# Kernel tuning notes

Measured on AMD Instinct MI355X. Metric: run time of the kernel, lower is better.

The kernel has to match this reference:

```python
import jax, jax.numpy as jnp
import numpy as np

B, T, M, D, H, DFF = 8, 512, 64, 1024, 16, 4096
DH = D // H          # 64 head dim
ROT = DH // 2        # 32 rotary dims (int(head_dim*0.5))
ROPE_BASE = 10000.0
LN_EPS = 1e-5


def layernorm(x, g, b):
    mu = jnp.mean(x, -1, keepdims=True)
    var = jnp.mean(jnp.square(x - mu), -1, keepdims=True)
    return (x - mu) * jax.lax.rsqrt(var + LN_EPS) * g + b


def rotate_half(x):
    x1, x2 = x[..., : x.shape[-1] // 2], x[..., x.shape[-1] // 2:]
    return jnp.concatenate((-x2, x1), -1)


def setup_inputs() -> dict:
    key = jax.random.key(0)
    ks = jax.random.split(key, 8)
    s = 0.02
    return {
        "x": jax.random.normal(ks[0], (B, T, D), jnp.float32),
        "memory": jax.random.normal(ks[1], (B, M, D), jnp.float32),
        "Wq": jax.random.normal(ks[2], (D, D), jnp.float32) * s,
        "bq": jnp.zeros((D,), jnp.float32),
        "Wk": jax.random.normal(ks[3], (D, D), jnp.float32) * s,
        "bk": jnp.zeros((D,), jnp.float32),
        "Wv": jax.random.normal(ks[4], (D, D), jnp.float32) * s,
        "bv": jnp.zeros((D,), jnp.float32),
        "Wo": jax.random.normal(ks[5], (D, D), jnp.float32) * s,
        "bo": jnp.zeros((D,), jnp.float32),
        "W1": jax.random.normal(ks[6], (DFF, D), jnp.float32) * s,
        "b1": jnp.zeros((DFF,), jnp.float32),
        "W2": jax.random.normal(ks[7], (D, DFF), jnp.float32) * s,
        "b2": jnp.zeros((D,), jnp.float32),
        "g_attn": jnp.ones((D,), jnp.float32),
        "beta_attn": jnp.zeros((D,), jnp.float32),
        "g_mlp": jnp.ones((D,), jnp.float32),
        "beta_mlp": jnp.zeros((D,), jnp.float32),
    }


def reference(x, memory, Wq, bq, Wk, bk, Wv, bv, Wo, bo, W1, b1, W2, b2,
              g_attn, beta_attn, g_mlp, beta_mlp):
    L = M + T
    x_full = jnp.concatenate([memory, x], axis=1)            # (B, L, D)
    xa = layernorm(x_full, g_attn, beta_attn)

    def heads(t):  # (B, L, D) -> (B, H, L, DH)
        return t.reshape(B, L, H, DH).transpose(0, 2, 1, 3)

    q = heads(xa @ Wq.T + bq)
    k = heads(xa @ Wk.T + bk)
    v = heads(xa @ Wv.T + bv)

    # partial rotary embedding on first ROT dims
    inv_freq = 1.0 / (ROPE_BASE ** (jnp.arange(0, ROT, 2, dtype=jnp.float32) / ROT))
    freqs = jnp.arange(L, dtype=jnp.float32)[:, None] * inv_freq[None, :]  # (L, ROT/2)
    emb = jnp.concatenate((freqs, freqs), -1)                # (L, ROT)
    cos = jnp.cos(emb)[None, None]                           # (1,1,L,ROT)
    sin = jnp.sin(emb)[None, None]
    q_rot, q_pass = q[..., :ROT], q[..., ROT:]
    k_rot, k_pass = k[..., :ROT], k[..., ROT:]
    q_rot = q_rot * cos + rotate_half(q_rot) * sin
    k_rot = k_rot * cos + rotate_half(k_rot) * sin
    q = jnp.concatenate((q_rot, q_pass), -1)
    k = jnp.concatenate((k_rot, k_pass), -1)

    # prompt mask: memory rows attend memory only; target rows attend memory + causal target
    idx = jnp.arange(L)
    row, col = idx[:, None], idx[None, :]
    allowed = (col < M) | ((row >= M) & (col <= row))        # (L, L) bool

    scores = jnp.einsum('bhqd,bhkd->bhqk', q, k) / jnp.sqrt(jnp.float32(DH))
    scores = jnp.where(allowed[None, None], scores, jnp.float32(-1e30))
    attn = jax.nn.softmax(scores, axis=-1)
    o = jnp.einsum('bhqk,bhkd->bhqd', attn, v)
    o = o.transpose(0, 2, 1, 3).reshape(B, L, D)
    x_full = x_full + (o @ Wo.T + bo)

    xn = layernorm(x_full, g_mlp, beta_mlp)
    h = jnp.square(jax.nn.relu(xn @ W1.T + b1))              # ReLU^2 FFN
    x_full = x_full + (h @ W2.T + b2)
    return x_full[:, M:]
```

## Files before the change

### kernel.cpp

```cpp
#include <hip/hip_runtime.h>
#include <hip/hip_bf16.h>
#include <cmath>

using bf16 = __hip_bfloat16;
typedef __attribute__((ext_vector_type(8))) __bf16 bf16x8;
typedef __attribute__((ext_vector_type(4))) float f32x4;

struct __align__(8) bf16x4s { bf16 a, b, c, d; };

__device__ inline void gload_lds16(const void* g, void* l) {
  __builtin_amdgcn_global_load_lds(
      (__attribute__((address_space(1))) void*)g,
      (__attribute__((address_space(3))) void*)l, 16, 0, 0);
}

__device__ inline f32x4 mfma16(bf16x8 a, bf16x8 b, f32x4 c) {
  return __builtin_amdgcn_mfma_f32_16x16x32_bf16(a, b, c, 0, 0, 0);
}

#define BAR() __builtin_amdgcn_s_barrier()
#define VMC(N) asm volatile("s_waitcnt vmcnt(" #N ")" ::: "memory")
#define LGKM0() asm volatile("s_waitcnt lgkmcnt(0)" ::: "memory")

template<int MODE, int CHUNK>
__global__ __launch_bounds__(512) void gemm256(
    const bf16* __restrict__ A, int lda, long sA,
    const bf16* __restrict__ B, int ldb, long sB,
    const float* __restrict__ bias,
    void* __restrict__ Out,
    int K, int ldo, long zstride)
{
  __shared__ bf16 lds[65536];
  const int tid = threadIdx.x, lane = tid & 63, wid = tid >> 6;
  const int wr = wid >> 2, wc = wid & 3;
  const int gx = gridDim.x;
  const int bidl = blockIdx.x + gx * blockIdx.y;
  const int xcd = bidl & 7, slot = bidl >> 3;
  int bx, by;
  if constexpr (CHUNK == 0) {
    const int sx = gx >> 2, sy = gridDim.y >> 1;
    bx = (xcd & 3) * sx + slot % sx;
    by = (xcd >> 2) * sy + slot / sx;
  } else {
    bx = slot % gx;
    by = xcd * (gridDim.y >> 3) + slot / gx;
  }
  const int m0 = by * 256, n0 = bx * 256;
  const int z = blockIdx.z;
  const bf16* Ab = A + (long)z * sA;
  const bf16* Bb = B + (long)z * sB;
  const int nt = K >> 6;

  f32x4 acc[8][4] = {};

  auto STAGE = [&](int par, int t, int part) {
    const bf16* src = (part < 2) ? Ab : Bb;
    const int ld = (part < 2) ? lda : ldb;
    const int rb = ((part < 2) ? m0 : n0) + (part & 1) * 128;
    const int k0 = t << 6;
    bf16* dst = &lds[(par * 4 + part) * 8192];
#pragma unroll
    for (int j = 0; j < 2; ++j) {
      int idx = j * 512 + tid;
      int row = idx >> 3;
      int ce = ((idx & 7) ^ (row & 7)) << 3;
      gload_lds16(src + (long)(rb + row) * ld + k0 + ce, dst + idx * 8);
    }
  };
  auto load_a = [&](bf16x8 (&a_)[4][2], int par, int mh) {
#pragma unroll
    for (int mf = 0; mf < 4; ++mf)
#pragma unroll
      for (int kk = 0; kk < 2; ++kk) {
        int r = mh * 64 + mf * 16 + (lane & 15);
        int cb = (kk * 64 + ((lane >> 4) << 4)) ^ ((r & 7) << 4);
        a_[mf][kk] = *(const bf16x8*)&lds[(par * 4 + wr) * 8192 + r * 64 + (cb >> 1)];
      }
  };
  auto load_b = [&](bf16x8 (&b_)[2][2], int par, int nh) {
#pragma unroll
    for (int nf = 0; nf < 2; ++nf)
#pragma unroll
      for (int kk = 0; kk < 2; ++kk) {
        int r = (wc & 1) * 64 + (nh * 2 + nf) * 16 + (lane & 15);
        int cb = (kk * 64 + ((lane >> 4) << 4)) ^ ((r & 7) << 4);
        b_[nf][kk] = *(const bf16x8*)&lds[(par * 4 + 2 + (wc >> 1)) * 8192 + r * 64 + (cb >> 1)];
      }
  };
  auto qmfma = [&](bf16x8 (&a_)[4][2], bf16x8 (&b_)[2][2], int mh, int nh) {
    __builtin_amdgcn_s_setprio(1);
#pragma unroll
    for (int mf = 0; mf < 4; ++mf)
#pragma unroll
      for (int nf = 0; nf < 2; ++nf)
#pragma unroll
        for (int kk = 0; kk < 2; ++kk)
          acc[mh * 4 + mf][nh * 2 + nf] =
              mfma16(a_[mf][kk], b_[nf][kk], acc[mh * 4 + mf][nh * 2 + nf]);
    __builtin_amdgcn_s_setprio(0);
  };

  STAGE(0, 0, 0); STAGE(0, 0, 1); STAGE(0, 0, 2); STAGE(0, 0, 3);
  STAGE(1, 1, 2); STAGE(1, 1, 0);
  VMC(4);
  BAR();

  const int half = nt >> 1;
  for (int i = 0; i < half; ++i) {
    const int u = 2 * i;
    const bool full = (i < half - 1);
    bf16x8 a[4][2], b0[2][2], b1[2][2];
    load_a(a, 0, 0); load_b(b0, 0, 0);
    STAGE(1, u + 1, 3);
    BAR();
    qmfma(a, b0, 0, 0);
    BAR();
    load_b(b1, 0, 1);
    STAGE(1, u + 1, 1);
    BAR();
    qmfma(a, b1, 0, 1);
    BAR();
    load_a(a, 0, 1);
    if (full) STAGE(0, u + 2, 2);
    BAR();
    qmfma(a, b1, 1, 1);
    BAR();
    if (full) STAGE(0, u + 2, 0);
    BAR();
    qmfma(a, b0, 1, 0);
    if (full) { VMC(4); } else { VMC(0); }
    BAR();
    load_a(a, 1, 0); load_b(b0, 1, 0);
    if (full) STAGE(0, u + 2, 3);
    BAR();
    qmfma(a, b0, 0, 0);
    BAR();
    load_b(b1, 1, 1);
    if (full) STAGE(0, u + 2, 1);
    BAR();
    qmfma(a, b1, 0, 1);
    BAR();
    load_a(a, 1, 1);
    if (full) STAGE(1, u + 3, 2);
    BAR();
    qmfma(a, b1, 1, 1);
    BAR();
    if (full) STAGE(1, u + 3, 0);
    BAR();
    qmfma(a, b0, 1, 0);
    if (full) VMC(4);
    BAR();
  }

  const int cb0 = n0 + wc * 64 + (lane & 15);
  const int rb0 = m0 + wr * 128 + ((lane >> 4) << 2);
#pragma unroll
  for (int mf = 0; mf < 8; ++mf) {
#pragma unroll
    for (int nf = 0; nf < 4; ++nf) {
      int c = cb0 + nf * 16;
#pragma unroll
      for (int j = 0; j < 4; ++j) {
        int rr = rb0 + mf * 16 + j;
        float v = acc[mf][nf][j];
        if constexpr (MODE == 0) {
          ((bf16*)Out)[(long)rr * ldo + c] = __float2bfloat16(v + bias[c]);
        } else if constexpr (MODE == 2) {
          float t2 = fmaxf(v + bias[c], 0.0f);
          ((bf16*)Out)[(long)rr * ldo + c] = __float2bfloat16(t2 * t2);
        } else {
          ((bf16*)Out)[(long)z * zstride + (long)rr * ldo + c] = __float2bfloat16(v);
        }
      }
    }
  }
}

__global__ __launch_bounds__(256) void reduce_k(
    const bf16* __restrict__ part, const float* __restrict__ bias,
    const float* __restrict__ resid, float* __restrict__ out)
{
  const int row = blockIdx.x, tid = threadIdx.x;
  const long rb = (long)row * 1024 + tid * 4;
  float a0 = 0, a1 = 0, a2 = 0, a3 = 0;
#pragma unroll
  for (int z = 0; z < 4; ++z) {
    bf16x4s t = *(const bf16x4s*)(part + (long)z * 4194304 + rb);
    a0 += __bfloat162float(t.a); a1 += __bfloat162float(t.b);
    a2 += __bfloat162float(t.c); a3 += __bfloat162float(t.d);
  }
  float4 b = ((const float4*)bias)[tid];
  float4 r = *(const float4*)(resid + rb);
  float4 o;
  o.x = a0 + b.x + r.x; o.y = a1 + b.y + r.y;
  o.z = a2 + b.z + r.z; o.w = a3 + b.w + r.w;
  *(float4*)(out + rb) = o;
}

__global__ __launch_bounds__(256) void reduce_ln(
    const bf16* __restrict__ part, const float* __restrict__ bias,
    const float* __restrict__ resid, const float* __restrict__ g,
    const float* __restrict__ beta, float* __restrict__ x2,
    bf16* __restrict__ xn)
{
  const int row = blockIdx.x, tid = threadIdx.x;
  const long rb = (long)row * 1024 + tid * 4;
  float a0 = 0, a1 = 0, a2 = 0, a3 = 0;
#pragma unroll
  for (int z = 0; z < 4; ++z) {
    bf16x4s t = *(const bf16x4s*)(part + (long)z * 4194304 + rb);
    a0 += __bfloat162float(t.a); a1 += __bfloat162float(t.b);
    a2 += __bfloat162float(t.c); a3 += __bfloat162float(t.d);
  }
  float4 bb4 = ((const float4*)bias)[tid];
  float4 rr4 = *(const float4*)(resid + rb);
  float4 v;
  v.x = a0 + bb4.x + rr4.x; v.y = a1 + bb4.y + rr4.y;
  v.z = a2 + bb4.z + rr4.z; v.w = a3 + bb4.w + rr4.w;
  *(float4*)(x2 + rb) = v;

  float s = v.x + v.y + v.z + v.w;
  float s2 = v.x * v.x + v.y * v.y + v.z * v.z + v.w * v.w;
#pragma unroll
  for (int o = 32; o; o >>= 1) {
    s += __shfl_down(s, o);
    s2 += __shfl_down(s2, o);
  }
  __shared__ float red[8];
  const int w = tid >> 6, lane = tid & 63;
  if (lane == 0) { red[w] = s; red[4 + w] = s2; }
  __syncthreads();
  float S = red[0] + red[1] + red[2] + red[3];
  float S2 = red[4] + red[5] + red[6] + red[7];
  float mu = S * (1.0f / 1024.0f);
  float rs = rsqrtf(S2 * (1.0f / 1024.0f) - mu * mu + 1e-5f);
  float4 gg = ((const float4*)g)[tid];
  float4 be = ((const float4*)beta)[tid];
  bf16x4s o4;
  o4.a = __float2bfloat16((v.x - mu) * rs * gg.x + be.x);
  o4.b = __float2bfloat16((v.y - mu) * rs * gg.y + be.y);
  o4.c = __float2bfloat16((v.z - mu) * rs * gg.z + be.z);
  o4.d = __float2bfloat16((v.w - mu) * rs * gg.w + be.w);
  *(bf16x4s*)(xn + rb) = o4;
}

__global__ __launch_bounds__(256) void flash_attn(
    const bf16* __restrict__ qh, const bf16* __restrict__ kh,
    const bf16* __restrict__ vt, bf16* __restrict__ attn)
{
  __shared__ bf16 ks[2][64 * 64];
  __shared__ bf16 vs[2][64 * 64];
  __shared__ bf16 pq[64 * 64];
  const int tid = threadIdx.x, lane = tid & 63, wv = tid >> 6;
  const int bid = blockIdx.x;
  const int xcd = bid & 7, sl = bid >> 3;
  const int zh = xcd * 16 + (sl >> 3);
  const int qt = sl & 7;
  const int b = zh >> 4, h = zh & 15;
  const int q0 = qt * 64;
  const bf16* qb = qh + (long)zh * 32768 + (long)q0 * 64;
  const bf16* kb = kh + (long)zh * 36864;
  const bf16* vb = vt + (long)zh * 36864;

#pragma unroll
  for (int i = 0; i < 2; ++i) {
    int idx = i * 256 + tid;
    int row = idx >> 3;
    int ce = ((idx & 7) ^ (row & 7)) << 3;
    gload_lds16(qb + (long)row * 64 + ce, pq + idx * 8);
  }
  auto stage_kv = [&](int bb, int j) {
#pragma unroll
    for (int it = 0; it < 2; ++it) {
      int idx = it * 256 + tid;
      int row = idx >> 3;
      int ce = ((idx & 7) ^ (row & 7)) << 3;
      gload_lds16(kb + (long)(j * 64 + row) * 64 + ce, &ks[bb][idx * 8]);
    }
#pragma unroll
    for (int it = 0; it < 2; ++it) {
      int idx = it * 256 + tid;
      int row = idx >> 3;
      int ce = ((idx & 7) ^ (row & 7)) << 3;
      gload_lds16(vb + (long)row * 576 + j * 64 + ce, &vs[bb][idx * 8]);
    }
  };
  stage_kv(0, 0);
  VMC(0);
  BAR();

  bf16x8 qf[2];
  {
    int r = wv * 16 + (lane & 15);
#pragma unroll
    for (int kk = 0; kk < 2; ++kk) {
      int c0 = kk * 32 + ((lane >> 4) << 3);
      qf[kk] = *(const bf16x8*)&pq[r * 64 + (c0 ^ ((r & 7) << 3))];
    }
  }

  f32x4 acc_o[4] = {};
  float mrun[4], lrun[4];
#pragma unroll
  for (int jj = 0; jj < 4; ++jj) { mrun[jj] = -1e30f; lrun[jj] = 0.0f; }

  const int nkv = qt + 2;
  int cur = 0;
  for (int j = 0; j < nkv; ++j) {
    if (j + 1 < nkv) stage_kv(cur ^ 1, j + 1);

    f32x4 sv[4] = {};
    __builtin_amdgcn_s_setprio(1);
#pragma unroll
    for (int kk = 0; kk < 2; ++kk) {
      bf16x8 kf[4];
      int c0 = kk * 32 + ((lane >> 4) << 3);
#pragma unroll
      for (int n = 0; n < 4; ++n) {
        int r = n * 16 + (lane & 15);
        kf[n] = *(const bf16x8*)&ks[cur][r * 64 + (c0 ^ ((r & 7) << 3))];
      }
#pragma unroll
      for (int n = 0; n < 4; ++n) sv[n] = mfma16(qf[kk], kf[n], sv[n]);
    }
    __builtin_amdgcn_s_setprio(0);

    if (j == nkv - 1) {
#pragma unroll
      for (int n = 0; n < 4; ++n) {
        int c = n * 16 + (lane & 15);
#pragma unroll
        for (int jj = 0; jj < 4; ++jj) {
          int r = wv * 16 + ((lane >> 4) << 2) + jj;
          if (c > r) sv[n][jj] = -1e30f;
        }
      }
    }
#pragma unroll
    for (int jj = 0; jj < 4; ++jj) {
      float pm = fmaxf(fmaxf(sv[0][jj], sv[1][jj]), fmaxf(sv[2][jj], sv[3][jj]));
#pragma unroll
      for (int off = 1; off < 16; off <<= 1) pm = fmaxf(pm, __shfl_xor(pm, off));
      float mnew = fmaxf(mrun[jj], pm);
      float sc = exp2f(mrun[jj] - mnew);
      mrun[jj] = mnew;
      float rs = 0.0f;
#pragma unroll
      for (int n = 0; n < 4; ++n) {
        float p = exp2f(sv[n][jj] - mnew);
        sv[n][jj] = p;
        rs += p;
      }
#pragma unroll
      for (int off = 1; off < 16; off <<= 1) rs += __shfl_xor(rs, off);
      lrun[jj] = lrun[jj] * sc + rs;
#pragma unroll
      for (int nd = 0; nd < 4; ++nd) acc_o[nd][jj] *= sc;
    }
#pragma unroll
    for (int n = 0; n < 4; ++n)
#pragma unroll
      for (int jj = 0; jj < 4; ++jj) {
        int pr = wv * 16 + ((lane >> 4) << 2) + jj;
        int pc = n * 16 + (lane & 15);
        pq[pr * 64 + (pc ^ ((pr & 7) << 3))] = __float2bfloat16(sv[n][jj]);
      }
    __builtin_amdgcn_s_setprio(1);
#pragma unroll
    for (int kk = 0; kk < 2; ++kk) {
      int c0 = kk * 32 + ((lane >> 4) << 3);
      bf16x8 pa, vf[4];
      {
        int r = wv * 16 + (lane & 15);
        pa = *(const bf16x8*)&pq[r * 64 + (c0 ^ ((r & 7) << 3))];
      }
#pragma unroll
      for (int nd = 0; nd < 4; ++nd) {
        int r = nd * 16 + (lane & 15);
        vf[nd] = *(const bf16x8*)&vs[cur][r * 64 + (c0 ^ ((r & 7) << 3))];
      }
#pragma unroll
      for (int nd = 0; nd < 4; ++nd) acc_o[nd] = mfma16(pa, vf[nd], acc_o[nd]);
    }
    __builtin_amdgcn_s_setprio(0);

    if (j + 1 < nkv) {
      LGKM0();
      VMC(0);
      BAR();
      cur ^= 1;
    }
  }
  bf16* ob = attn + ((long)b * 512 + q0) * 1024 + h * 64;
#pragma unroll
  for (int jj = 0; jj < 4; ++jj) {
    float inv = 1.0f / lrun[jj];
    int r = wv * 16 + ((lane >> 4) << 2) + jj;
#pragma unroll
    for (int nd = 0; nd < 4; ++nd)
      ob[(long)r * 1024 + nd * 16 + (lane & 15)] = __float2bfloat16(acc_o[nd][jj] * inv);
  }
}

template<bool CONCAT>
__global__ __launch_bounds__(256) void ln_kernel(
    const float* __restrict__ xin, const float* __restrict__ mem,
    const float* __restrict__ g, const float* __restrict__ beta,
    bf16* __restrict__ out)
{
  const int row = blockIdx.x;
  const float* src;
  if (CONCAT) {
    int b = row / 576, p = row % 576;
    src = (p < 64) ? (mem + ((long)b * 64 + p) * 1024)
                   : (xin + ((long)b * 512 + (p - 64)) * 1024);
  } else {
    src = xin + (long)row * 1024;
  }
  const int tid = threadIdx.x;
  float4 v = ((const float4*)src)[tid];
  float s = v.x + v.y + v.z + v.w;
  float s2 = v.x * v.x + v.y * v.y + v.z * v.z + v.w * v.w;
#pragma unroll
  for (int o = 32; o; o >>= 1) {
    s += __shfl_down(s, o);
    s2 += __shfl_down(s2, o);
  }
  __shared__ float red[8];
  const int w = tid >> 6, lane = tid & 63;
  if (lane == 0) { red[w] = s; red[4 + w] = s2; }
  __syncthreads();
  float S = red[0] + red[1] + red[2] + red[3];
  float S2 = red[4] + red[5] + red[6] + red[7];
  float mu = S * (1.0f / 1024.0f);
  float rs = rsqrtf(S2 * (1.0f / 1024.0f) - mu * mu + 1e-5f);
  float4 gg = ((const float4*)g)[tid];
  float4 bb = ((const float4*)beta)[tid];
  bf16x4s o4;
  o4.a = __float2bfloat16((v.x - mu) * rs * gg.x + bb.x);
  o4.b = __float2bfloat16((v.y - mu) * rs * gg.y + bb.y);
  o4.c = __float2bfloat16((v.z - mu) * rs * gg.z + bb.z);
  o4.d = __float2bfloat16((v.w - mu) * rs * gg.w + bb.w);
  *(bf16x4s*)(out + (long)row * 1024 + tid * 4) = o4;
}

__global__ __launch_bounds__(256) void cvt_weights(
    const float* __restrict__ wq, const float* __restrict__ wk,
    const float* __restrict__ wv, const float* __restrict__ wo,
    const float* __restrict__ w1, const float* __restrict__ w2,
    bf16* __restrict__ out)
{
  long e = ((long)blockIdx.x * 256 + threadIdx.x) * 4;
  const long DD = 1048576, DF = 4194304;
  const float* src; long base;
  if (e < DD)            { src = wq; base = 0; }
  else if (e < 2 * DD)   { src = wk; base = DD; }
  else if (e < 3 * DD)   { src = wv; base = 2 * DD; }
  else if (e < 4 * DD)   { src = wo; base = 3 * DD; }
  else if (e < 4 * DD + DF) { src = w1; base = 4 * DD; }
  else                   { src = w2; base = 4 * DD + DF; }
  float4 v = *(const float4*)(src + (e - base));
  bf16x4s o4;
  o4.a = __float2bfloat16(v.x);
  o4.b = __float2bfloat16(v.y);
  o4.c = __float2bfloat16(v.z);
  o4.d = __float2bfloat16(v.w);
  *(bf16x4s*)(out + e) = o4;
}

__global__ __launch_bounds__(256) void bias_concat(
    const float* __restrict__ bq, const float* __restrict__ bk,
    const float* __restrict__ bv, float* __restrict__ out)
{
  int i = blockIdx.x * 256 + threadIdx.x;
  if (i < 1024)      out[i] = bq[i];
  else if (i < 2048) out[i] = bk[i - 1024];
  else if (i < 3072) out[i] = bv[i - 2048];
}

__global__ __launch_bounds__(256) void rope_tab_kernel(float* __restrict__ tab)
{
  int i = blockIdx.x * 256 + threadIdx.x;
  if (i >= 9216) return;
  int p = i >> 4, f = i & 15;
  float invf = expf(-(float)f * 0.5756462732485114f);
  float ang = (float)p * invf;
  tab[i] = cosf(ang);
  tab[9216 + i] = sinf(ang);
}

__global__ __launch_bounds__(256) void rope_reshape(
    const bf16* __restrict__ qkv, const float* __restrict__ tab,
    bf16* __restrict__ qh, bf16* __restrict__ kh, bf16* __restrict__ vt)
{
  const float QSCALE = 0.18033688011112043f;
  long i = (long)blockIdx.x * 256 + threadIdx.x;
  if (i >= 8L * 576 * 1024) return;
  int dfull = (int)(i & 1023);
  long bp = i >> 10;
  int p = (int)(bp % 576);
  int b = (int)(bp / 576);
  int h = dfull >> 6, d = dfull & 63;
  const bf16* rowp = qkv + bp * 3072;

  float cosv = 1.0f, sinv = 0.0f;
  const bool rot = d < 32;
  int pd = 0;
  if (rot) {
    int i0 = d & 15;
    cosv = tab[p * 16 + i0];
    sinv = tab[9216 + p * 16 + i0];
    pd = (d < 16) ? d + 16 : d - 16;
  }
  {
    float v0 = __bfloat162float(rowp[1024 + dfull]);
    float ov = v0;
    if (rot) {
      float v1 = __bfloat162float(rowp[1024 + (h << 6) + pd]);
      ov = (d < 16) ? (v0 * cosv - v1 * sinv) : (v0 * cosv + v1 * sinv);
    }
    kh[(((long)b * 16 + h) * 576 + p) * 64 + d] = __float2bfloat16(ov);
  }
  vt[(((long)b * 16 + h) * 64 + d) * 576 + p] = rowp[2048 + dfull];
  if (p >= 64) {
    float v0 = __bfloat162float(rowp[dfull]);
    float ov = v0;
    if (rot) {
      float v1 = __bfloat162float(rowp[(h << 6) + pd]);
      ov = (d < 16) ? (v0 * cosv - v1 * sinv) : (v0 * cosv + v1 * sinv);
    }
    qh[(((long)b * 16 + h) * 512 + (p - 64)) * 64 + d] = __float2bfloat16(ov * QSCALE);
  }
}

extern "C" void kernel_launch(void* const* d_in, const int* in_sizes, int n_in,
                              void* d_out, int out_size, void* d_ws, size_t ws_size,
                              hipStream_t stream)
{
  (void)in_sizes; (void)n_in; (void)out_size; (void)ws_size;
  const float* x    = (const float*)d_in[0];
  const float* mem  = (const float*)d_in[1];
  const float* Wq   = (const float*)d_in[2];
  const float* bq   = (const float*)d_in[3];
  const float* Wk   = (const float*)d_in[4];
  const float* bk   = (const float*)d_in[5];
  const float* Wv   = (const float*)d_in[6];
  const float* bv   = (const float*)d_in[7];
  const float* Wo   = (const float*)d_in[8];
  const float* bo   = (const float*)d_in[9];
  const float* W1   = (const float*)d_in[10];
  const float* b1   = (const float*)d_in[11];
  const float* W2   = (const float*)d_in[12];
  const float* b2   = (const float*)d_in[13];
  const float* g_a  = (const float*)d_in[14];
  const float* bt_a = (const float*)d_in[15];
  const float* g_m  = (const float*)d_in[16];
  const float* bt_m = (const float*)d_in[17];
  float* out = (float*)d_out;

  char* ws = (char*)d_ws;
  size_t off = 0;
  auto carve = [&](size_t bytes) -> void* {
    void* p = ws + off;
    off = (off + bytes + 255) & ~(size_t)255;
    return p;
  };
  bf16*  wB    = (bf16*)carve(12582912L * 2);
  float* bqkv  = (float*)carve(3072 * 4);
  float* rtab  = (float*)carve(9216 * 2 * 4);
  bf16*  xa    = (bf16*)carve(4608L * 1024 * 2);
  bf16*  qkv   = (bf16*)carve(4608L * 3072 * 2);
  bf16*  qh    = (bf16*)carve(8L * 16 * 512 * 64 * 2);
  bf16*  kh    = (bf16*)carve(8L * 16 * 576 * 64 * 2);
  bf16*  vt    = (bf16*)carve(8L * 16 * 576 * 64 * 2);
  bf16*  attn  = (bf16*)carve(4096L * 1024 * 2);
  float* x2    = (float*)carve(4096L * 1024 * 4);
  bf16*  xn    = (bf16*)carve(4096L * 1024 * 2);
  bf16*  hbuf  = (bf16*)carve(4096L * 4096 * 2);
  bf16*  partsb= (bf16*)carve(4L * 4096 * 1024 * 2);

  cvt_weights<<<12288, 256, 0, stream>>>(Wq, Wk, Wv, Wo, W1, W2, wB);
  bias_concat<<<12, 256, 0, stream>>>(bq, bk, bv, bqkv);
  rope_tab_kernel<<<36, 256, 0, stream>>>(rtab);
  ln_kernel<true><<<4608, 256, 0, stream>>>(x, mem, g_a, bt_a, xa);

  gemm256<0, 0><<<dim3(12, 18, 1), 512, 0, stream>>>(
      xa, 1024, 0, wB, 1024, 0, bqkv, qkv, 1024, 3072, 0);

  rope_reshape<<<18432, 256, 0, stream>>>(qkv, rtab, qh, kh, vt);

  flash_attn<<<1024, 256, 0, stream>>>(qh, kh, vt, attn);

  gemm256<8, 1><<<dim3(4, 16, 4), 512, 0, stream>>>(
      attn, 1024, 256, wB + 3145728L, 1024, 256, nullptr, partsb, 256, 1024, 4194304L);
  reduce_ln<<<4096, 256, 0, stream>>>(partsb, bo, x, g_m, bt_m, x2, xn);

  gemm256<2, 0><<<dim3(16, 16, 1), 512, 0, stream>>>(
      xn, 1024, 0, wB + 4194304L, 1024, 0, b1, hbuf, 1024, 4096, 0);

  gemm256<8, 1><<<dim3(4, 16, 4), 512, 0, stream>>>(
      hbuf, 4096, 1024, wB + 8388608L, 4096, 1024, nullptr, partsb, 1024, 1024, 4194304L);
  reduce_k<<<4096, 256, 0, stream>>>(partsb, b2, x2, out);
}
```

Baseline: 241.9 us.

## Fuse RoPE and head reshape into QKV GEMM epilogue, stage stores through LDS

The QKV projection GEMM now applies bias, rotary embedding and the Q scale in its epilogue and writes Q, K and row-major V straight into per-head layouts. This drops the intermediate qkv buffer and the separate rope_reshape pass. A small tiled v_transpose kernel then produces the transposed V. All GEMM epilogues now stage results through swizzled LDS and emit 16-byte vector stores instead of scattered 2-byte stores. The cost is extra LDS traffic and a barrier in the epilogue, plus one added kernel launch.

```diff
diff --git a/kernel.cpp b/kernel.cpp
--- a/kernel.cpp
+++ b/kernel.cpp
@@ -28,22 +28,24 @@
     const bf16* __restrict__ B, int ldb, long sB,
     const float* __restrict__ bias,
     void* __restrict__ Out,
-    int K, int ldo, long zstride)
+    int K, int ldo, long zstride,
+    const float* __restrict__ rtab,
+    bf16* __restrict__ o1, bf16* __restrict__ o2, bf16* __restrict__ o3)
 {
   __shared__ bf16 lds[65536];
   const int tid = threadIdx.x, lane = tid & 63, wid = tid >> 6;
   const int wr = wid >> 2, wc = wid & 3;
   const int gx = gridDim.x;
   const int bidl = blockIdx.x + gx * blockIdx.y;
-  const int xcd = bidl & 7, slot = bidl >> 3;
+  const int xcd = bidl & 7, slot_ = bidl >> 3;
   int bx, by;
   if constexpr (CHUNK == 0) {
     const int sx = gx >> 2, sy = gridDim.y >> 1;
-    bx = (xcd & 3) * sx + slot % sx;
-    by = (xcd >> 2) * sy + slot / sx;
+    bx = (xcd & 3) * sx + slot_ % sx;
+    by = (xcd >> 2) * sy + slot_ / sx;
   } else {
-    bx = slot % gx;
-    by = xcd * (gridDim.y >> 3) + slot / gx;
+    bx = slot_ % gx;
+    by = xcd * (gridDim.y >> 3) + slot_ / gx;
   }
   const int m0 = by * 256, n0 = bx * 256;
   const int z = blockIdx.z;
@@ -152,26 +154,74 @@
     BAR();
   }
 
-  const int cb0 = n0 + wc * 64 + (lane & 15);
-  const int rb0 = m0 + wr * 128 + ((lane >> 4) << 2);
+  bf16* slot = &lds[wid * 8192];
+  const int l15 = lane & 15;
+  const int matq = n0 >> 10;
+  const int hh = ((n0 & 1023) >> 6) + wc;
+  float b0v = 0, b1v = 0, b2v = 0, b3v = 0;
+  if constexpr (MODE != 8) {
+    b0v = bias[n0 + wc * 64 + l15];
+    b1v = bias[n0 + wc * 64 + l15 + 16];
+    b2v = bias[n0 + wc * 64 + l15 + 32];
+    b3v = bias[n0 + wc * 64 + l15 + 48];
+  }
 #pragma unroll
   for (int mf = 0; mf < 8; ++mf) {
 #pragma unroll
-    for (int nf = 0; nf < 4; ++nf) {
-      int c = cb0 + nf * 16;
-#pragma unroll
-      for (int j = 0; j < 4; ++j) {
-        int rr = rb0 + mf * 16 + j;
-        float v = acc[mf][nf][j];
-        if constexpr (MODE == 0) {
-          ((bf16*)Out)[(long)rr * ldo + c] = __float2bfloat16(v + bias[c]);
-        } else if constexpr (MODE == 2) {
-          float t2 = fmaxf(v + bias[c], 0.0f);
-          ((bf16*)Out)[(long)rr * ldo + c] = __float2bfloat16(t2 * t2);
-        } else {
-          ((bf16*)Out)[(long)z * zstride + (long)rr * ldo + c] = __float2bfloat16(v);
+    for (int j = 0; j < 4; ++j) {
+      int lr = mf * 16 + ((lane >> 4) << 2) + j;
+      float a0 = acc[mf][0][j] + b0v;
+      float a1 = acc[mf][1][j] + b1v;
+      float a2 = acc[mf][2][j] + b2v;
+      float a3 = acc[mf][3][j] + b3v;
+      if constexpr (MODE == 9) {
+        if (matq < 2) {
+          int rr = m0 + wr * 128 + lr;
+          int p = rr % 576;
+          float cs = rtab[p * 16 + l15];
+          float sn = rtab[9216 + p * 16 + l15];
+          float r0 = a0 * cs - a1 * sn;
+          float r1 = a1 * cs + a0 * sn;
+          a0 = r0; a1 = r1;
+          if (matq == 0) {
+            const float QS = 0.18033688011112043f;
+            a0 *= QS; a1 *= QS; a2 *= QS; a3 *= QS;
+          }
         }
-      }
+      } else if constexpr (MODE == 2) {
+        a0 = fmaxf(a0, 0.f); a0 *= a0;
+        a1 = fmaxf(a1, 0.f); a1 *= a1;
+        a2 = fmaxf(a2, 0.f); a2 *= a2;
+        a3 = fmaxf(a3, 0.f); a3 *= a3;
+      }
+      int sw = (lr & 7) << 3;
+      slot[lr * 64 + ((l15) ^ sw)]        = __float2bfloat16(a0);
+      slot[lr * 64 + ((l15 + 16) ^ sw)]   = __float2bfloat16(a1);
+      slot[lr * 64 + ((l15 + 32) ^ sw)]   = __float2bfloat16(a2);
+      slot[lr * 64 + ((l15 + 48) ^ sw)]   = __float2bfloat16(a3);
+    }
+  }
+  __syncthreads();
+#pragma unroll
+  for (int it = 0; it < 16; ++it) {
+    int u = it * 64 + lane;
+    int r_s = u >> 3, c_s = u & 7;
+    int rr = m0 + wr * 128 + r_s;
+    bf16x8 val = *(const bf16x8*)&slot[r_s * 64 + ((c_s ^ (r_s & 7)) << 3)];
+    if constexpr (MODE == 9) {
+      int b_ = rr / 576, p = rr - b_ * 576;
+      int zh = b_ * 16 + hh;
+      if (matq == 0) {
+        if (p >= 64)
+          *(bf16x8*)(o1 + ((long)zh * 512 + (p - 64)) * 64 + c_s * 8) = val;
+      } else if (matq == 1) {
+        *(bf16x8*)(o2 + ((long)zh * 576 + p) * 64 + c_s * 8) = val;
+      } else {
+        *(bf16x8*)(o3 + ((long)zh * 576 + p) * 64 + c_s * 8) = val;
+      }
+    } else {
+      long zoff = (MODE == 8) ? (long)z * zstride : 0;
+      *(bf16x8*)((bf16*)Out + zoff + (long)rr * ldo + n0 + wc * 64 + c_s * 8) = val;
     }
   }
 }
@@ -244,6 +294,32 @@
   *(bf16x4s*)(xn + rb) = o4;
 }
 
+__global__ __launch_bounds__(256) void v_transpose(
+    const bf16* __restrict__ vrow, bf16* __restrict__ vt)
+{
+  __shared__ bf16 t[64][72];
+  const int tid = threadIdx.x;
+  const int zh = blockIdx.y, pb = blockIdx.x;
+  const bf16* src = vrow + ((long)zh * 576 + pb * 64) * 64;
+#pragma unroll
+  for (int it = 0; it < 2; ++it) {
+    int idx = it * 256 + tid;
+    int r = idx >> 3, c0 = (idx & 7) << 3;
+    *(bf16x8*)&t[r][c0] = *(const bf16x8*)&src[r * 64 + c0];
+  }
+  __syncthreads();
+  bf16* dst = vt + (long)zh * 36864 + pb * 64;
+#pragma unroll
+  for (int it = 0; it < 2; ++it) {
+    int idx = it * 256 + tid;
+    int d = idx >> 3, p0 = (idx & 7) << 3;
+    bf16 tmp[8] __attribute__((aligned(16)));
+#pragma unroll
+    for (int k = 0; k < 8; ++k) tmp[k] = t[p0 + k][d];
+    *(bf16x8*)&dst[(long)d * 576 + p0] = *(const bf16x8*)&tmp[0];
+  }
+}
+
 __global__ __launch_bounds__(256) void flash_attn(
     const bf16* __restrict__ qh, const bf16* __restrict__ kh,
     const bf16* __restrict__ vt, bf16* __restrict__ attn)
@@ -487,50 +563,6 @@
   float ang = (float)p * invf;
   tab[i] = cosf(ang);
   tab[9216 + i] = sinf(ang);
-}
-
-__global__ __launch_bounds__(256) void rope_reshape(
-    const bf16* __restrict__ qkv, const float* __restrict__ tab,
-    bf16* __restrict__ qh, bf16* __restrict__ kh, bf16* __restrict__ vt)
-{
-  const float QSCALE = 0.18033688011112043f;
-  long i = (long)blockIdx.x * 256 + threadIdx.x;
-  if (i >= 8L * 576 * 1024) return;
-  int dfull = (int)(i & 1023);
-  long bp = i >> 10;
-  int p = (int)(bp % 576);
-  int b = (int)(bp / 576);
-  int h = dfull >> 6, d = dfull & 63;
-  const bf16* rowp = qkv + bp * 3072;
-
-  float cosv = 1.0f, sinv = 0.0f;
-  const bool rot = d < 32;
-  int pd = 0;
-  if (rot) {
-    int i0 = d & 15;
-    cosv = tab[p * 16 + i0];
-    sinv = tab[9216 + p * 16 + i0];
-    pd = (d < 16) ? d + 16 : d - 16;
-  }
-  {
-    float v0 = __bfloat162float(rowp[1024 + dfull]);
-    float ov = v0;
-    if (rot) {
-      float v1 = __bfloat162float(rowp[1024 + (h << 6) + pd]);
-      ov = (d < 16) ? (v0 * cosv - v1 * sinv) : (v0 * cosv + v1 * sinv);
-    }
-    kh[(((long)b * 16 + h) * 576 + p) * 64 + d] = __float2bfloat16(ov);
-  }
-  vt[(((long)b * 16 + h) * 64 + d) * 576 + p] = rowp[2048 + dfull];
-  if (p >= 64) {
-    float v0 = __bfloat162float(rowp[dfull]);
-    float ov = v0;
-    if (rot) {
-      float v1 = __bfloat162float(rowp[(h << 6) + pd]);
-      ov = (d < 16) ? (v0 * cosv - v1 * sinv) : (v0 * cosv + v1 * sinv);
-    }
-    qh[(((long)b * 16 + h) * 512 + (p - 64)) * 64 + d] = __float2bfloat16(ov * QSCALE);
-  }
 }
 
 extern "C" void kernel_launch(void* const* d_in, const int* in_sizes, int n_in,
@@ -569,9 +601,9 @@
   float* bqkv  = (float*)carve(3072 * 4);
   float* rtab  = (float*)carve(9216 * 2 * 4);
   bf16*  xa    = (bf16*)carve(4608L * 1024 * 2);
-  bf16*  qkv   = (bf16*)carve(4608L * 3072 * 2);
   bf16*  qh    = (bf16*)carve(8L * 16 * 512 * 64 * 2);
   bf16*  kh    = (bf16*)carve(8L * 16 * 576 * 64 * 2);
+  bf16*  vrow  = (bf16*)carve(8L * 16 * 576 * 64 * 2);
   bf16*  vt    = (bf16*)carve(8L * 16 * 576 * 64 * 2);
   bf16*  attn  = (bf16*)carve(4096L * 1024 * 2);
   float* x2    = (float*)carve(4096L * 1024 * 4);
@@ -584,21 +616,25 @@
   rope_tab_kernel<<<36, 256, 0, stream>>>(rtab);
   ln_kernel<true><<<4608, 256, 0, stream>>>(x, mem, g_a, bt_a, xa);
 
-  gemm256<0, 0><<<dim3(12, 18, 1), 512, 0, stream>>>(
-      xa, 1024, 0, wB, 1024, 0, bqkv, qkv, 1024, 3072, 0);
-
-  rope_reshape<<<18432, 256, 0, stream>>>(qkv, rtab, qh, kh, vt);
+  gemm256<9, 0><<<dim3(12, 18, 1), 512, 0, stream>>>(
+      xa, 1024, 0, wB, 1024, 0, bqkv, nullptr, 1024, 0, 0,
+      rtab, qh, kh, vrow);
+
+  v_transpose<<<dim3(9, 128), 256, 0, stream>>>(vrow, vt);
 
   flash_attn<<<1024, 256, 0, stream>>>(qh, kh, vt, attn);
 
   gemm256<8, 1><<<dim3(4, 16, 4), 512, 0, stream>>>(
-      attn, 1024, 256, wB + 3145728L, 1024, 256, nullptr, partsb, 256, 1024, 4194304L);
+      attn, 1024, 256, wB + 3145728L, 1024, 256, nullptr, partsb, 256, 1024,
+      4194304L, nullptr, nullptr, nullptr, nullptr);
   reduce_ln<<<4096, 256, 0, stream>>>(partsb, bo, x, g_m, bt_m, x2, xn);
 
   gemm256<2, 0><<<dim3(16, 16, 1), 512, 0, stream>>>(
-      xn, 1024, 0, wB + 4194304L, 1024, 0, b1, hbuf, 1024, 4096, 0);
+      xn, 1024, 0, wB + 4194304L, 1024, 0, b1, hbuf, 1024, 4096, 0,
+      nullptr, nullptr, nullptr, nullptr);
 
   gemm256<8, 1><<<dim3(4, 16, 4), 512, 0, stream>>>(
-      hbuf, 4096, 1024, wB + 8388608L, 4096, 1024, nullptr, partsb, 1024, 1024, 4194304L);
+      hbuf, 4096, 1024, wB + 8388608L, 4096, 1024, nullptr, partsb, 1024, 1024,
+      4194304L, nullptr, nullptr, nullptr, nullptr);
   reduce_k<<<4096, 256, 0, stream>>>(partsb, b2, x2, out);
 }
```

Measured after the change: 224.7 us. 1.08x faster.
